# Kernel tuning notes

Hardware: AMD Instinct MI355X
Metric: run time of the kernel (lower is better)

## Reference

```python
import jax, jax.numpy as jnp
import numpy as np

GAMMA = 20.0
GAMMA2 = 10.0
KATZ_FACTOR = 0.999
EPS = 1e-12


def setup_inputs() -> dict:
    key = jax.random.key(0)
    k1, k2 = jax.random.split(key)
    b, n_way, k_shot, q, c, h, w = 32, 5, 5, 75, 640, 5, 5
    support_xf = jax.random.normal(k1, (b, n_way * k_shot, c, h, w), dtype=jnp.float32)
    query_xf = jax.random.normal(k2, (b, q, c, h, w), dtype=jnp.float32)
    return {"support_xf": support_xf, "query_xf": query_xf, "n_way": n_way, "k_shot": k_shot}


def _l2norm(x, axis):
    return x * jax.lax.rsqrt(jnp.sum(x * x, axis=axis, keepdims=True) + EPS)


def reference(support_xf, query_xf, n_way, k_shot):
    b, s, c, h, w = support_xf.shape
    q = query_xf.shape[1]
    hw = h * w
    # prototype support features: mean over shots -> (b, n_way, c, hw)
    sup = support_xf.reshape(b, n_way, k_shot, c, hw).mean(axis=2)
    qry = query_xf.reshape(b, q, c, hw)
    # cosine similarity between every query location and every support location
    sup_n = _l2norm(sup, axis=2)   # (b, n, c, hw)
    qry_n = _l2norm(qry, axis=2)   # (b, q, c, hw)
    # S[b,q,i,n,k]: query pos i vs support (class n, pos k) -> (b*q, M_q, M_s)
    M_q, M_s = hw, n_way * hw
    N = b * q
    S = jnp.einsum('bqci,bnck->bqink', qry_n, sup_n).reshape(N, M_q, M_s)
    # double softmax transition blocks
    T_sq = jax.nn.softmax(GAMMA * S, axis=-1)                    # (N, M_q, M_s)
    T_qs = jax.nn.softmax(GAMMA2 * S.transpose(0, 2, 1), axis=-1)  # (N, M_s, M_q)
    # bipartite block transition matrix T (N, M_s+M_q, M_s+M_q)
    top = jnp.concatenate(
        [jnp.zeros((N, M_s, M_s), S.dtype), T_sq.transpose(0, 2, 1)], axis=-1)
    bot = jnp.concatenate(
        [T_qs.transpose(0, 2, 1), jnp.zeros((N, M_q, M_q), S.dtype)], axis=-1)
    T = jnp.concatenate([top, bot], axis=-2)
    M = M_s + M_q
    eye = jnp.eye(M, dtype=S.dtype)
    ones = jnp.ones((N, M, 1), S.dtype)
    # katz = (inv(I - kT) - I) @ 1 == solve(I - kT, 1) - 1
    katz = (jnp.linalg.solve(eye[None] - KATZ_FACTOR * T, ones) - ones).squeeze(-1)
    kq = katz[:, M_s:]
    ks = katz[:, :M_s]
    katz_query = kq / kq.sum(-1, keepdims=True)
    katz_support = ks / ks.sum(-1, keepdims=True)
    katz_support = katz_support.reshape(b, q, n_way, hw)
    katz_support = katz_support / katz_support.sum(-1, keepdims=True)
    katz_support = katz_support.reshape(b, q, n_way, 1, h, w)
    katz_query = katz_query.reshape(b, q, 1, h, w)
    return (katz_query, katz_support)
```

## Files before the change

kernel.cpp:

```cpp
#include <hip/hip_runtime.h>

namespace {
constexpr int CH = 640, HW = 25, MS = 125;
constexpr int CHW = CH * HW;
constexpr float GAMMA = 20.f, GAMMA2 = 10.f;
constexpr float EPS = 1e-12f;
}

__global__ __launch_bounds__(256)
void prep_sup128_kernel(const float* __restrict__ sup, float* __restrict__ supt) {
  __shared__ __align__(16) float m[CHW];
  __shared__ float inv[HW];
  const int bn = blockIdx.x;
  const int b = bn / 5, n = bn % 5;
  const float* base = sup + ((size_t)b * 25 + n * 5) * CHW;
  for (int idx = threadIdx.x; idx < CHW; idx += 256) {
    float s = 0.f;
    #pragma unroll
    for (int sh = 0; sh < 5; ++sh) s += base[sh * CHW + idx];
    m[idx] = s * 0.2f;
  }
  __syncthreads();
  {
    int i = threadIdx.x >> 3, s8 = threadIdx.x & 7;
    if (i < HW) {
      float p = 0.f;
      for (int c = s8; c < CH; c += 8) { float v = m[c * HW + i]; p += v * v; }
      p += __shfl_xor(p, 1); p += __shfl_xor(p, 2); p += __shfl_xor(p, 4);
      if (s8 == 0) inv[i] = rsqrtf(p + EPS);
    }
  }
  __syncthreads();
  float* ob = supt + (size_t)b * (CH * 128);
  for (int idx = threadIdx.x; idx < CHW; idx += 256) {
    int c = idx / 25, i = idx - c * 25;
    ob[c * 128 + n * 25 + i] = m[idx] * inv[i];
  }
  if (n == 0)
    for (int c = threadIdx.x; c < CH; c += 256) {
      ob[c * 128 + 125] = 0.f; ob[c * 128 + 126] = 0.f; ob[c * 128 + 127] = 0.f;
    }
}

__global__ __launch_bounds__(256)
void prep_sup_kernel(const float* __restrict__ sup, float* __restrict__ sup_t) {
  __shared__ __align__(16) float m[CHW];
  __shared__ float inv[HW];
  const int bn = blockIdx.x;
  const float* base = sup + (size_t)(bn / 5) * (25 * CHW) + (size_t)(bn % 5) * (5 * CHW);
  for (int idx = threadIdx.x; idx < CHW; idx += 256) {
    float s = 0.f;
    #pragma unroll
    for (int sh = 0; sh < 5; ++sh) s += base[sh * CHW + idx];
    m[idx] = s * 0.2f;
  }
  __syncthreads();
  {
    int i = threadIdx.x >> 3, s8 = threadIdx.x & 7;
    if (i < HW) {
      float p = 0.f;
      for (int c = s8; c < CH; c += 8) { float v = m[c * HW + i]; p += v * v; }
      p += __shfl_xor(p, 1); p += __shfl_xor(p, 2); p += __shfl_xor(p, 4);
      if (s8 == 0) inv[i] = rsqrtf(p + EPS);
    }
  }
  __syncthreads();
  float* outp = sup_t + (size_t)bn * CHW;
  for (int idx = threadIdx.x; idx < CHW; idx += 256) {
    int k = idx / CH, c = idx - k * CH;
    outp[idx] = m[c * HW + k] * inv[k];
  }
}

__global__ __launch_bounds__(256)
void gemm_s_kernel(const float* __restrict__ qry, const float* __restrict__ sup128,
                   float* __restrict__ Sout) {
  __shared__ __align__(16) float atile[2][16 * 128];
  __shared__ __align__(16) float btile[2][16 * 128];
  __shared__ float invq_s[128];

  const int tid = threadIdx.x;
  const int wid = tid >> 6, lane = tid & 63;
  const int Bl = (blockIdx.x & 7) * 60 + (blockIdx.x >> 3);
  const int b = Bl / 15, qg = Bl - 15 * b;
  const float* qbase = qry + ((size_t)b * 75 + (size_t)qg * 5) * CHW;
  const float* sb = sup128 + (size_t)b * (CH * 128);
  const int ty = tid >> 4, tx = tid & 15;

  const int row0 = lane;
  const int qq0 = row0 / 25, i0 = row0 - 25 * qq0;
  int row1 = 64 + lane; if (row1 > 124) row1 = 124;
  const int qq1 = row1 / 25, i1 = row1 - 25 * qq1;
  const size_t aoff0 = (size_t)qq0 * CHW + i0;
  const size_t aoff1 = (size_t)qq1 * CHW + i1;

  auto STAGE = [&](int pp, int c0) {
    float* at = atile[pp];
    float* bt = btile[pp];
    #pragma unroll
    for (int rr = 0; rr < 8; ++rr) {
      const int r = 8 * wid + rr;
      const int k = r >> 1;
      const size_t aoff = (r & 1) ? aoff1 : aoff0;
      const float* src = qbase + aoff + (size_t)(c0 + k) * 25;
      __builtin_amdgcn_global_load_lds(
          (const __attribute__((address_space(1))) void*)src,
          (__attribute__((address_space(3))) void*)(at + r * 64), 4, 0, 0);
    }
    #pragma unroll
    for (int jj = 0; jj < 2; ++jj) {
      const int j = 2 * wid + jj;
      const float* src = sb + (size_t)(c0 + 2 * j) * 128 + lane * 4;
      __builtin_amdgcn_global_load_lds(
          (const __attribute__((address_space(1))) void*)src,
          (__attribute__((address_space(3))) void*)(bt + j * 256), 16, 0, 0);
    }
  };

  float acc[2][2][4][4];
  #pragma unroll
  for (int g = 0; g < 2; ++g)
    #pragma unroll
    for (int h = 0; h < 2; ++h)
      #pragma unroll
      for (int u = 0; u < 4; ++u)
        #pragma unroll
        for (int v = 0; v < 4; ++v) acc[g][h][u][v] = 0.f;
  float npart = 0.f;

  STAGE(0, 0);
  asm volatile("s_waitcnt vmcnt(0)" ::: "memory");
  __syncthreads();

  int p = 0;
  for (int t = 0; t < 40; ++t) {
    if (t < 39) STAGE(p ^ 1, 16 * (t + 1));
    const float* at = atile[p];
    const float* bt = btile[p];
    if (tid < MS) {
      #pragma unroll
      for (int k = 0; k < 16; ++k) { float v = at[k * 128 + tid]; npart += v * v; }
    }
    #pragma unroll
    for (int k = 0; k < 16; ++k) {
      const float4 a0 = *(const float4*)&at[k * 128 + 4 * ty];
      const float4 a1 = *(const float4*)&at[k * 128 + 64 + 4 * ty];
      const float4 b0 = *(const float4*)&bt[k * 128 + 4 * tx];
      const float4 b1 = *(const float4*)&bt[k * 128 + 64 + 4 * tx];
      const float ag[2][4] = {{a0.x, a0.y, a0.z, a0.w}, {a1.x, a1.y, a1.z, a1.w}};
      const float bg[2][4] = {{b0.x, b0.y, b0.z, b0.w}, {b1.x, b1.y, b1.z, b1.w}};
      #pragma unroll
      for (int g = 0; g < 2; ++g)
        #pragma unroll
        for (int u = 0; u < 4; ++u)
          #pragma unroll
          for (int h = 0; h < 2; ++h)
            #pragma unroll
            for (int v = 0; v < 4; ++v) acc[g][h][u][v] += ag[g][u] * bg[h][v];
    }
    asm volatile("s_waitcnt vmcnt(0)" ::: "memory");
    __syncthreads();
    p ^= 1;
  }
  if (tid < MS) invq_s[tid] = rsqrtf(npart + EPS);
  __syncthreads();

  float* Sg = Sout + (size_t)(b * 75 + qg * 5) * 3200;
  #pragma unroll
  for (int g = 0; g < 2; ++g)
    #pragma unroll
    for (int u = 0; u < 4; ++u) {
      const int row = g * 64 + 4 * ty + u;
      if (row < MS) {
        const float iv = invq_s[row];
        const int qq = row / 25, r = row - 25 * qq;
        #pragma unroll
        for (int h = 0; h < 2; ++h) {
          float4 val;
          val.x = acc[g][h][u][0] * iv;
          val.y = acc[g][h][u][1] * iv;
          val.z = acc[g][h][u][2] * iv;
          val.w = acc[g][h][u][3] * iv;
          *(float4*)(Sg + (size_t)qq * 3200 + r * 128 + h * 64 + 4 * tx) = val;
        }
      }
    }
}

__global__ __launch_bounds__(256)
void solve_kernel(const float* __restrict__ Sg, float* __restrict__ out) {
  __shared__ float Sld[25 * 131];
  __shared__ float Qm[3125];
  __shared__ double Msol[675];
  __shared__ double xsd[HW];
  __shared__ float kqs[HW];
  __shared__ float ksf[MS];

  const int tid = threadIdx.x;
  const int bq = blockIdx.x;
  const float* src = Sg + (size_t)bq * 3200;
  for (int idx = tid; idx < 3200; idx += 256) {
    const int row = idx >> 7, c = idx & 127;
    Sld[row * 131 + c] = src[idx];
  }
  __syncthreads();

  if (tid < MS) {
    float mx = -1e30f;
    #pragma unroll
    for (int i = 0; i < HW; ++i) mx = fmaxf(mx, Sld[i * 131 + tid]);
    float e[HW]; float sum = 0.f;
    #pragma unroll
    for (int i = 0; i < HW; ++i) { e[i] = __expf(GAMMA2 * (Sld[i * 131 + tid] - mx)); sum += e[i]; }
    float is = 1.f / sum;
    #pragma unroll
    for (int i = 0; i < HW; ++i) Qm[tid * HW + i] = e[i] * is;
  }
  __syncthreads();

  {
    int i = tid >> 3, s8 = tid & 7;
    if (i < HW) {
      float mx = -1e30f;
      for (int j = s8; j < MS; j += 8) mx = fmaxf(mx, Sld[i * 131 + j]);
      mx = fmaxf(mx, __shfl_xor(mx, 1));
      mx = fmaxf(mx, __shfl_xor(mx, 2));
      mx = fmaxf(mx, __shfl_xor(mx, 4));
      float sum = 0.f;
      for (int j = s8; j < MS; j += 8) {
        float e = __expf(GAMMA * (Sld[i * 131 + j] - mx));
        Sld[i * 131 + j] = e; sum += e;
      }
      sum += __shfl_xor(sum, 1); sum += __shfl_xor(sum, 2); sum += __shfl_xor(sum, 4);
      float is = 1.f / sum;
      for (int j = s8; j < MS; j += 8) Sld[i * 131 + j] *= is;
    }
  }
  __syncthreads();

  #pragma unroll
  for (int t = 0; t < 3; ++t) {
    const int pp = tid + 256 * t;
    if (pp < 650) {
      const int i = pp / 26, i2 = pp - 26 * i;
      float s = 0.f;
      if (i2 < 25) {
        for (int j = 0; j < MS; ++j) s += Qm[j * HW + i] * Sld[i2 * 131 + j];
        Msol[i * 27 + i2] = (i == i2 ? 1.0 : 0.0) - 0.998001 * (double)s;
      } else {
        for (int j = 0; j < MS; ++j) s += Qm[j * HW + i];
        Msol[i * 27 + 25] = 1.0 + 0.999 * (double)s;
      }
    }
  }
  __syncthreads();

  for (int k = 0; k < 24; ++k) {
    const double invp = 1.0 / Msol[k * 27 + k];
    const int jj = k + 1 + (tid & 31);
    for (int i = k + 1 + (tid >> 5); i < HW; i += 8) {
      const double f = Msol[i * 27 + k] * invp;
      if (jj <= HW) Msol[i * 27 + jj] -= f * Msol[k * 27 + jj];
    }
    __syncthreads();
  }
  for (int k = 24; k >= 0; --k) {
    const double xk = Msol[k * 27 + 25] / Msol[k * 27 + k];
    if (tid == 0) xsd[k] = xk;
    if (tid < k) Msol[tid * 27 + 25] -= Msol[tid * 27 + k] * xk;
    __syncthreads();
  }

  if (tid < HW) kqs[tid] = (float)(xsd[tid] - 1.0);
  if (tid < MS) {
    float a = 0.f;
    #pragma unroll
    for (int i = 0; i < HW; ++i) a += Sld[i * 131 + tid] * (float)xsd[i];
    ksf[tid] = 0.999f * a;
  }
  __syncthreads();
  if (tid < HW) {
    float s = 0.f;
    #pragma unroll
    for (int i = 0; i < HW; ++i) s += kqs[i];
    out[(size_t)bq * HW + tid] = kqs[tid] / s;
  }
  if (tid < MS) {
    const int n = tid / HW;
    float s = 0.f;
    #pragma unroll
    for (int k2 = 0; k2 < HW; ++k2) s += ksf[n * HW + k2];
    out[60000 + (size_t)bq * MS + tid] = ksf[tid] / s;
  }
}

__global__ __launch_bounds__(256)
void melmask_kernel(const float* __restrict__ qry, const float* __restrict__ sup_t,
                    float* __restrict__ out) {
  __shared__ __align__(16) float pool[4224];
  __shared__ __align__(16) float Sld[3125];
  __shared__ double Msol[675];
  __shared__ double xsd[HW];
  __shared__ float invq_s[128];
  __shared__ float kqs[HW];
  __shared__ float ksf[MS];

  float* atile = pool;
  float* btile = pool + 2112;
  float* Qm    = pool;

  const int tid = threadIdx.x;
  const int Bl = (blockIdx.x & 7) * 60 + (blockIdx.x >> 3);
  const int b = Bl / 15, qg = Bl - 15 * b;
  const float* qbase = qry + ((size_t)b * 75 + (size_t)qg * 5) * CHW;
  const float* sbase = sup_t + (size_t)b * (MS * CH);
  const int ty = tid >> 4, tx = tid & 15;

  float acc[2][2][4][4];
  #pragma unroll
  for (int g = 0; g < 2; ++g)
    #pragma unroll
    for (int h = 0; h < 2; ++h)
      #pragma unroll
      for (int u = 0; u < 4; ++u)
        #pragma unroll
        for (int v = 0; v < 4; ++v) acc[g][h][u][v] = 0.f;
  float npart = 0.f;

  for (int c0 = 0; c0 < CH; c0 += 16) {
    __syncthreads();
    #pragma unroll
    for (int mm = 0; mm < 8; ++mm) {
      int idx = tid + 256 * mm;
      int k = idx >> 7, row = idx & 127;
      float v = 0.f;
      if (row < MS) {
        int qq = row / 25, i = row - 25 * qq;
        v = qbase[(size_t)qq * CHW + (size_t)(c0 + k) * 25 + i];
      }
      atile[k * 132 + row] = v;
    }
    #pragma unroll
    for (int mm = 0; mm < 2; ++mm) {
      int idx = tid + 256 * mm;
      int col = idx >> 2, kq = idx & 3;
      float4 v = make_float4(0.f, 0.f, 0.f, 0.f);
      if (col < MS) v = *(const float4*)(sbase + (size_t)col * CH + c0 + 4 * kq);
      btile[(4 * kq + 0) * 132 + col] = v.x;
      btile[(4 * kq + 1) * 132 + col] = v.y;
      btile[(4 * kq + 2) * 132 + col] = v.z;
      btile[(4 * kq + 3) * 132 + col] = v.w;
    }
    __syncthreads();
    if (tid < MS) {
      #pragma unroll
      for (int k = 0; k < 16; ++k) { float v = atile[k * 132 + tid]; npart += v * v; }
    }
    #pragma unroll
    for (int k = 0; k < 16; ++k) {
      const float4 a0 = *(const float4*)&atile[k * 132 + 4 * ty];
      const float4 a1 = *(const float4*)&atile[k * 132 + 64 + 4 * ty];
      const float4 b0 = *(const float4*)&btile[k * 132 + 4 * tx];
      const float4 b1 = *(const float4*)&btile[k * 132 + 64 + 4 * tx];
      const float ag[2][4] = {{a0.x, a0.y, a0.z, a0.w}, {a1.x, a1.y, a1.z, a1.w}};
      const float bg[2][4] = {{b0.x, b0.y, b0.z, b0.w}, {b1.x, b1.y, b1.z, b1.w}};
      #pragma unroll
      for (int g = 0; g < 2; ++g)
        #pragma unroll
        for (int u = 0; u < 4; ++u)
          #pragma unroll
          for (int h = 0; h < 2; ++h)
            #pragma unroll
            for (int v = 0; v < 4; ++v) acc[g][h][u][v] += ag[g][u] * bg[h][v];
    }
  }
  if (tid < MS) invq_s[tid] = rsqrtf(npart + EPS);
  __syncthreads();

  for (int qq = 0; qq < 5; ++qq) {
    const int bq = b * 75 + qg * 5 + qq;
    const int r0 = qq * 25;
    #pragma unroll
    for (int g = 0; g < 2; ++g)
      #pragma unroll
      for (int u = 0; u < 4; ++u) {
        const int row = g * 64 + 4 * ty + u;
        if (row >= r0 && row < r0 + 25) {
          const int r = row - r0;
          const float iv = invq_s[row];
          #pragma unroll
          for (int h = 0; h < 2; ++h)
            #pragma unroll
            for (int v = 0; v < 4; ++v) {
              const int col = h * 64 + 4 * tx + v;
              if (col < MS) Sld[r * MS + col] = acc[g][h][u][v] * iv;
            }
        }
      }
    __syncthreads();
    if (tid < MS) {
      float mx = -1e30f;
      #pragma unroll
      for (int i = 0; i < HW; ++i) mx = fmaxf(mx, Sld[i * MS + tid]);
      float e[HW]; float sum = 0.f;
      #pragma unroll
      for (int i = 0; i < HW; ++i) { e[i] = __expf(GAMMA2 * (Sld[i * MS + tid] - mx)); sum += e[i]; }
      float is = 1.f / sum;
      #pragma unroll
      for (int i = 0; i < HW; ++i) Qm[tid * HW + i] = e[i] * is;
    }
    __syncthreads();
    {
      int i = tid >> 3, s8 = tid & 7;
      if (i < HW) {
        float mx = -1e30f;
        for (int j = s8; j < MS; j += 8) mx = fmaxf(mx, Sld[i * MS + j]);
        mx = fmaxf(mx, __shfl_xor(mx, 1));
        mx = fmaxf(mx, __shfl_xor(mx, 2));
        mx = fmaxf(mx, __shfl_xor(mx, 4));
        float sum = 0.f;
        for (int j = s8; j < MS; j += 8) {
          float e = __expf(GAMMA * (Sld[i * MS + j] - mx));
          Sld[i * MS + j] = e; sum += e;
        }
        sum += __shfl_xor(sum, 1); sum += __shfl_xor(sum, 2); sum += __shfl_xor(sum, 4);
        float is = 1.f / sum;
        for (int j = s8; j < MS; j += 8) Sld[i * MS + j] *= is;
      }
    }
    __syncthreads();
    float* P = Sld;
    #pragma unroll
    for (int t = 0; t < 3; ++t) {
      const int pp = tid + 256 * t;
      if (pp < 650) {
        const int i = pp / 26, i2 = pp - 26 * i;
        float s = 0.f;
        if (i2 < 25) {
          for (int j = 0; j < MS; ++j) s += Qm[j * HW + i] * P[i2 * MS + j];
          Msol[i * 27 + i2] = (i == i2 ? 1.0 : 0.0) - 0.998001 * (double)s;
        } else {
          for (int j = 0; j < MS; ++j) s += Qm[j * HW + i];
          Msol[i * 27 + 25] = 1.0 + 0.999 * (double)s;
        }
      }
    }
    __syncthreads();
    for (int k = 0; k < 24; ++k) {
      const double invp = 1.0 / Msol[k * 27 + k];
      const int jj = k + 1 + (tid & 31);
      for (int i = k + 1 + (tid >> 5); i < HW; i += 8) {
        const double f = Msol[i * 27 + k] * invp;
        if (jj <= HW) Msol[i * 27 + jj] -= f * Msol[k * 27 + jj];
      }
      __syncthreads();
    }
    for (int k = 24; k >= 0; --k) {
      const double xk = Msol[k * 27 + 25] / Msol[k * 27 + k];
      if (tid == 0) xsd[k] = xk;
      if (tid < k) Msol[tid * 27 + 25] -= Msol[tid * 27 + k] * xk;
      __syncthreads();
    }
    if (tid < HW) kqs[tid] = (float)(xsd[tid] - 1.0);
    if (tid < MS) {
      float a = 0.f;
      #pragma unroll
      for (int i = 0; i < HW; ++i) a += P[i * MS + tid] * (float)xsd[i];
      ksf[tid] = 0.999f * a;
    }
    __syncthreads();
    if (tid < HW) {
      float s = 0.f;
      #pragma unroll
      for (int i = 0; i < HW; ++i) s += kqs[i];
      out[(size_t)bq * HW + tid] = kqs[tid] / s;
    }
    if (tid < MS) {
      const int n = tid / HW;
      float s = 0.f;
      #pragma unroll
      for (int k2 = 0; k2 < HW; ++k2) s += ksf[n * HW + k2];
      out[60000 + (size_t)bq * MS + tid] = ksf[tid] / s;
    }
    __syncthreads();
  }
}

extern "C" void kernel_launch(void* const* d_in, const int* in_sizes, int n_in,
                              void* d_out, int out_size, void* d_ws, size_t ws_size,
                              hipStream_t stream) {
  const float* sup = (const float*)d_in[0];
  const float* qry = (const float*)d_in[1];
  float* outp = (float*)d_out;
  const size_t sup128_bytes = (size_t)32 * CH * 128 * 4;
  const size_t sg_bytes = (size_t)2400 * 3200 * 4;
  if (ws_size >= sup128_bytes + sg_bytes) {
    float* sup128 = (float*)d_ws;
    float* Sg = (float*)((char*)d_ws + sup128_bytes);
    prep_sup128_kernel<<<160, 256, 0, stream>>>(sup, sup128);
    gemm_s_kernel<<<480, 256, 0, stream>>>(qry, sup128, Sg);
    solve_kernel<<<2400, 256, 0, stream>>>(Sg, outp);
  } else {
    float* sup_t = (float*)d_ws;
    prep_sup_kernel<<<160, 256, 0, stream>>>(sup, sup_t);
    melmask_kernel<<<480, 256, 0, stream>>>(qry, sup_t, outp);
  }
}
```

Baseline: 243.1 us.

## Split GEMM reduction over channels into two halves to double block count

The similarity GEMM is split along the 640-channel reduction into two halves, so 960 blocks run instead of 480. Each half writes its partial S and partial query-norm sums to separate workspace buffers. The solve kernel then adds the two partials and applies the inverse norm before the existing softmax and solve steps. This is meant to raise occupancy on a GPU with many CUs, at the cost of extra workspace traffic and a larger workspace requirement. The old fused melmask fallback is removed and the non-split gemm path becomes the fallback.

```diff
diff --git a/kernel.cpp b/kernel.cpp
--- a/kernel.cpp
+++ b/kernel.cpp
@@ -43,33 +43,118 @@
 }
 
 __global__ __launch_bounds__(256)
-void prep_sup_kernel(const float* __restrict__ sup, float* __restrict__ sup_t) {
-  __shared__ __align__(16) float m[CHW];
-  __shared__ float inv[HW];
-  const int bn = blockIdx.x;
-  const float* base = sup + (size_t)(bn / 5) * (25 * CHW) + (size_t)(bn % 5) * (5 * CHW);
-  for (int idx = threadIdx.x; idx < CHW; idx += 256) {
-    float s = 0.f;
-    #pragma unroll
-    for (int sh = 0; sh < 5; ++sh) s += base[sh * CHW + idx];
-    m[idx] = s * 0.2f;
-  }
-  __syncthreads();
-  {
-    int i = threadIdx.x >> 3, s8 = threadIdx.x & 7;
-    if (i < HW) {
-      float p = 0.f;
-      for (int c = s8; c < CH; c += 8) { float v = m[c * HW + i]; p += v * v; }
-      p += __shfl_xor(p, 1); p += __shfl_xor(p, 2); p += __shfl_xor(p, 4);
-      if (s8 == 0) inv[i] = rsqrtf(p + EPS);
-    }
-  }
-  __syncthreads();
-  float* outp = sup_t + (size_t)bn * CHW;
-  for (int idx = threadIdx.x; idx < CHW; idx += 256) {
-    int k = idx / CH, c = idx - k * CH;
-    outp[idx] = m[c * HW + k] * inv[k];
-  }
+void gemm_ks_kernel(const float* __restrict__ qry, const float* __restrict__ sup128,
+                    float* __restrict__ Sg1, float* __restrict__ Sg2,
+                    float* __restrict__ npws) {
+  __shared__ __align__(16) float atile[2][16 * 128];
+  __shared__ __align__(16) float btile[2][16 * 128];
+
+  const int tid = threadIdx.x;
+  const int wid = tid >> 6, lane = tid & 63;
+  const int x = blockIdx.x & 7, rr0 = blockIdx.x >> 3;
+  const int Bl = x * 120 + rr0;
+  const int group = Bl >> 1, half = Bl & 1;
+  const int b = group / 15, qg = group - 15 * b;
+  const float* qbase = qry + ((size_t)b * 75 + (size_t)qg * 5) * CHW;
+  const float* sb = sup128 + (size_t)b * (CH * 128);
+  const int ty = tid >> 4, tx = tid & 15;
+  const int kbase = half * 320;
+
+  const int row0 = lane;
+  const int qq0 = row0 / 25, i0 = row0 - 25 * qq0;
+  int row1 = 64 + lane; if (row1 > 124) row1 = 124;
+  const int qq1 = row1 / 25, i1 = row1 - 25 * qq1;
+  const size_t aoff0 = (size_t)qq0 * CHW + i0;
+  const size_t aoff1 = (size_t)qq1 * CHW + i1;
+
+  auto STAGE = [&](int pp, int c0) {
+    float* at = atile[pp];
+    float* bt = btile[pp];
+    #pragma unroll
+    for (int rr = 0; rr < 8; ++rr) {
+      const int r = 8 * wid + rr;
+      const int k = r >> 1;
+      const size_t aoff = (r & 1) ? aoff1 : aoff0;
+      const float* src = qbase + aoff + (size_t)(c0 + k) * 25;
+      __builtin_amdgcn_global_load_lds(
+          (const __attribute__((address_space(1))) void*)src,
+          (__attribute__((address_space(3))) void*)(at + r * 64), 4, 0, 0);
+    }
+    #pragma unroll
+    for (int jj = 0; jj < 2; ++jj) {
+      const int j = 2 * wid + jj;
+      const float* src = sb + (size_t)(c0 + 2 * j) * 128 + lane * 4;
+      __builtin_amdgcn_global_load_lds(
+          (const __attribute__((address_space(1))) void*)src,
+          (__attribute__((address_space(3))) void*)(bt + j * 256), 16, 0, 0);
+    }
+  };
+
+  float acc[2][2][4][4];
+  #pragma unroll
+  for (int g = 0; g < 2; ++g)
+    #pragma unroll
+    for (int h = 0; h < 2; ++h)
+      #pragma unroll
+      for (int u = 0; u < 4; ++u)
+        #pragma unroll
+        for (int v = 0; v < 4; ++v) acc[g][h][u][v] = 0.f;
+  float npart = 0.f;
+
+  STAGE(0, kbase);
+  asm volatile("s_waitcnt vmcnt(0)" ::: "memory");
+  __syncthreads();
+
+  int p = 0;
+  for (int t = 0; t < 20; ++t) {
+    if (t < 19) STAGE(p ^ 1, kbase + 16 * (t + 1));
+    const float* at = atile[p];
+    const float* bt = btile[p];
+    if (tid < MS) {
+      #pragma unroll
+      for (int k = 0; k < 16; ++k) { float v = at[k * 128 + tid]; npart += v * v; }
+    }
+    #pragma unroll
+    for (int k = 0; k < 16; ++k) {
+      const float4 a0 = *(const float4*)&at[k * 128 + 4 * ty];
+      const float4 a1 = *(const float4*)&at[k * 128 + 64 + 4 * ty];
+      const float4 b0 = *(const float4*)&bt[k * 128 + 4 * tx];
+      const float4 b1 = *(const float4*)&bt[k * 128 + 64 + 4 * tx];
+      const float ag[2][4] = {{a0.x, a0.y, a0.z, a0.w}, {a1.x, a1.y, a1.z, a1.w}};
+      const float bg[2][4] = {{b0.x, b0.y, b0.z, b0.w}, {b1.x, b1.y, b1.z, b1.w}};
+      #pragma unroll
+      for (int g = 0; g < 2; ++g)
+        #pragma unroll
+        for (int u = 0; u < 4; ++u)
+          #pragma unroll
+          for (int h = 0; h < 2; ++h)
+            #pragma unroll
+            for (int v = 0; v < 4; ++v) acc[g][h][u][v] += ag[g][u] * bg[h][v];
+    }
+    asm volatile("s_waitcnt vmcnt(0)" ::: "memory");
+    __syncthreads();
+    p ^= 1;
+  }
+
+  if (tid < MS) npws[(size_t)(group * 2 + half) * 128 + tid] = npart;
+
+  float* Sg = (half ? Sg2 : Sg1) + (size_t)(group * 5) * 3200;
+  #pragma unroll
+  for (int g = 0; g < 2; ++g)
+    #pragma unroll
+    for (int u = 0; u < 4; ++u) {
+      const int row = g * 64 + 4 * ty + u;
+      if (row < MS) {
+        const int qq = row / 25, r = row - 25 * qq;
+        #pragma unroll
+        for (int h = 0; h < 2; ++h) {
+          float4 val;
+          val.x = acc[g][h][u][0]; val.y = acc[g][h][u][1];
+          val.z = acc[g][h][u][2]; val.w = acc[g][h][u][3];
+          *(float4*)(Sg + (size_t)qq * 3200 + r * 128 + h * 64 + 4 * tx) = val;
+        }
+      }
+    }
 }
 
 __global__ __launch_bounds__(256)
@@ -187,24 +272,9 @@
     }
 }
 
-__global__ __launch_bounds__(256)
-void solve_kernel(const float* __restrict__ Sg, float* __restrict__ out) {
-  __shared__ float Sld[25 * 131];
-  __shared__ float Qm[3125];
-  __shared__ double Msol[675];
-  __shared__ double xsd[HW];
-  __shared__ float kqs[HW];
-  __shared__ float ksf[MS];
-
-  const int tid = threadIdx.x;
-  const int bq = blockIdx.x;
-  const float* src = Sg + (size_t)bq * 3200;
-  for (int idx = tid; idx < 3200; idx += 256) {
-    const int row = idx >> 7, c = idx & 127;
-    Sld[row * 131 + c] = src[idx];
-  }
-  __syncthreads();
-
+__device__ __forceinline__
+void solve_body(float* Sld, float* Qm, double* Msol, double* xsd,
+                float* kqs, float* ksf, int tid, int bq, float* out) {
   if (tid < MS) {
     float mx = -1e30f;
     #pragma unroll
@@ -295,195 +365,53 @@
 }
 
 __global__ __launch_bounds__(256)
-void melmask_kernel(const float* __restrict__ qry, const float* __restrict__ sup_t,
-                    float* __restrict__ out) {
-  __shared__ __align__(16) float pool[4224];
-  __shared__ __align__(16) float Sld[3125];
+void solve_ks_kernel(const float* __restrict__ Sg1, const float* __restrict__ Sg2,
+                     const float* __restrict__ npws, float* __restrict__ out) {
+  __shared__ float Sld[25 * 131];
+  __shared__ float Qm[3125];
   __shared__ double Msol[675];
   __shared__ double xsd[HW];
-  __shared__ float invq_s[128];
   __shared__ float kqs[HW];
   __shared__ float ksf[MS];
-
-  float* atile = pool;
-  float* btile = pool + 2112;
-  float* Qm    = pool;
+  __shared__ float ivrow[32];
 
   const int tid = threadIdx.x;
-  const int Bl = (blockIdx.x & 7) * 60 + (blockIdx.x >> 3);
-  const int b = Bl / 15, qg = Bl - 15 * b;
-  const float* qbase = qry + ((size_t)b * 75 + (size_t)qg * 5) * CHW;
-  const float* sbase = sup_t + (size_t)b * (MS * CH);
-  const int ty = tid >> 4, tx = tid & 15;
-
-  float acc[2][2][4][4];
-  #pragma unroll
-  for (int g = 0; g < 2; ++g)
-    #pragma unroll
-    for (int h = 0; h < 2; ++h)
-      #pragma unroll
-      for (int u = 0; u < 4; ++u)
-        #pragma unroll
-        for (int v = 0; v < 4; ++v) acc[g][h][u][v] = 0.f;
-  float npart = 0.f;
-
-  for (int c0 = 0; c0 < CH; c0 += 16) {
-    __syncthreads();
-    #pragma unroll
-    for (int mm = 0; mm < 8; ++mm) {
-      int idx = tid + 256 * mm;
-      int k = idx >> 7, row = idx & 127;
-      float v = 0.f;
-      if (row < MS) {
-        int qq = row / 25, i = row - 25 * qq;
-        v = qbase[(size_t)qq * CHW + (size_t)(c0 + k) * 25 + i];
-      }
-      atile[k * 132 + row] = v;
-    }
-    #pragma unroll
-    for (int mm = 0; mm < 2; ++mm) {
-      int idx = tid + 256 * mm;
-      int col = idx >> 2, kq = idx & 3;
-      float4 v = make_float4(0.f, 0.f, 0.f, 0.f);
-      if (col < MS) v = *(const float4*)(sbase + (size_t)col * CH + c0 + 4 * kq);
-      btile[(4 * kq + 0) * 132 + col] = v.x;
-      btile[(4 * kq + 1) * 132 + col] = v.y;
-      btile[(4 * kq + 2) * 132 + col] = v.z;
-      btile[(4 * kq + 3) * 132 + col] = v.w;
-    }
-    __syncthreads();
-    if (tid < MS) {
-      #pragma unroll
-      for (int k = 0; k < 16; ++k) { float v = atile[k * 132 + tid]; npart += v * v; }
-    }
-    #pragma unroll
-    for (int k = 0; k < 16; ++k) {
-      const float4 a0 = *(const float4*)&atile[k * 132 + 4 * ty];
-      const float4 a1 = *(const float4*)&atile[k * 132 + 64 + 4 * ty];
-      const float4 b0 = *(const float4*)&btile[k * 132 + 4 * tx];
-      const float4 b1 = *(const float4*)&btile[k * 132 + 64 + 4 * tx];
-      const float ag[2][4] = {{a0.x, a0.y, a0.z, a0.w}, {a1.x, a1.y, a1.z, a1.w}};
-      const float bg[2][4] = {{b0.x, b0.y, b0.z, b0.w}, {b1.x, b1.y, b1.z, b1.w}};
-      #pragma unroll
-      for (int g = 0; g < 2; ++g)
-        #pragma unroll
-        for (int u = 0; u < 4; ++u)
-          #pragma unroll
-          for (int h = 0; h < 2; ++h)
-            #pragma unroll
-            for (int v = 0; v < 4; ++v) acc[g][h][u][v] += ag[g][u] * bg[h][v];
-    }
-  }
-  if (tid < MS) invq_s[tid] = rsqrtf(npart + EPS);
-  __syncthreads();
-
-  for (int qq = 0; qq < 5; ++qq) {
-    const int bq = b * 75 + qg * 5 + qq;
-    const int r0 = qq * 25;
-    #pragma unroll
-    for (int g = 0; g < 2; ++g)
-      #pragma unroll
-      for (int u = 0; u < 4; ++u) {
-        const int row = g * 64 + 4 * ty + u;
-        if (row >= r0 && row < r0 + 25) {
-          const int r = row - r0;
-          const float iv = invq_s[row];
-          #pragma unroll
-          for (int h = 0; h < 2; ++h)
-            #pragma unroll
-            for (int v = 0; v < 4; ++v) {
-              const int col = h * 64 + 4 * tx + v;
-              if (col < MS) Sld[r * MS + col] = acc[g][h][u][v] * iv;
-            }
-        }
-      }
-    __syncthreads();
-    if (tid < MS) {
-      float mx = -1e30f;
-      #pragma unroll
-      for (int i = 0; i < HW; ++i) mx = fmaxf(mx, Sld[i * MS + tid]);
-      float e[HW]; float sum = 0.f;
-      #pragma unroll
-      for (int i = 0; i < HW; ++i) { e[i] = __expf(GAMMA2 * (Sld[i * MS + tid] - mx)); sum += e[i]; }
-      float is = 1.f / sum;
-      #pragma unroll
-      for (int i = 0; i < HW; ++i) Qm[tid * HW + i] = e[i] * is;
-    }
-    __syncthreads();
-    {
-      int i = tid >> 3, s8 = tid & 7;
-      if (i < HW) {
-        float mx = -1e30f;
-        for (int j = s8; j < MS; j += 8) mx = fmaxf(mx, Sld[i * MS + j]);
-        mx = fmaxf(mx, __shfl_xor(mx, 1));
-        mx = fmaxf(mx, __shfl_xor(mx, 2));
-        mx = fmaxf(mx, __shfl_xor(mx, 4));
-        float sum = 0.f;
-        for (int j = s8; j < MS; j += 8) {
-          float e = __expf(GAMMA * (Sld[i * MS + j] - mx));
-          Sld[i * MS + j] = e; sum += e;
-        }
-        sum += __shfl_xor(sum, 1); sum += __shfl_xor(sum, 2); sum += __shfl_xor(sum, 4);
-        float is = 1.f / sum;
-        for (int j = s8; j < MS; j += 8) Sld[i * MS + j] *= is;
-      }
-    }
-    __syncthreads();
-    float* P = Sld;
-    #pragma unroll
-    for (int t = 0; t < 3; ++t) {
-      const int pp = tid + 256 * t;
-      if (pp < 650) {
-        const int i = pp / 26, i2 = pp - 26 * i;
-        float s = 0.f;
-        if (i2 < 25) {
-          for (int j = 0; j < MS; ++j) s += Qm[j * HW + i] * P[i2 * MS + j];
-          Msol[i * 27 + i2] = (i == i2 ? 1.0 : 0.0) - 0.998001 * (double)s;
-        } else {
-          for (int j = 0; j < MS; ++j) s += Qm[j * HW + i];
-          Msol[i * 27 + 25] = 1.0 + 0.999 * (double)s;
-        }
-      }
-    }
-    __syncthreads();
-    for (int k = 0; k < 24; ++k) {
-      const double invp = 1.0 / Msol[k * 27 + k];
-      const int jj = k + 1 + (tid & 31);
-      for (int i = k + 1 + (tid >> 5); i < HW; i += 8) {
-        const double f = Msol[i * 27 + k] * invp;
-        if (jj <= HW) Msol[i * 27 + jj] -= f * Msol[k * 27 + jj];
-      }
-      __syncthreads();
-    }
-    for (int k = 24; k >= 0; --k) {
-      const double xk = Msol[k * 27 + 25] / Msol[k * 27 + k];
-      if (tid == 0) xsd[k] = xk;
-      if (tid < k) Msol[tid * 27 + 25] -= Msol[tid * 27 + k] * xk;
-      __syncthreads();
-    }
-    if (tid < HW) kqs[tid] = (float)(xsd[tid] - 1.0);
-    if (tid < MS) {
-      float a = 0.f;
-      #pragma unroll
-      for (int i = 0; i < HW; ++i) a += P[i * MS + tid] * (float)xsd[i];
-      ksf[tid] = 0.999f * a;
-    }
-    __syncthreads();
-    if (tid < HW) {
-      float s = 0.f;
-      #pragma unroll
-      for (int i = 0; i < HW; ++i) s += kqs[i];
-      out[(size_t)bq * HW + tid] = kqs[tid] / s;
-    }
-    if (tid < MS) {
-      const int n = tid / HW;
-      float s = 0.f;
-      #pragma unroll
-      for (int k2 = 0; k2 < HW; ++k2) s += ksf[n * HW + k2];
-      out[60000 + (size_t)bq * MS + tid] = ksf[tid] / s;
-    }
-    __syncthreads();
-  }
+  const int bq = blockIdx.x;
+  const int g5 = bq / 5, qq = bq - 5 * g5;
+  if (tid < HW) {
+    const float n1 = npws[(size_t)(g5 * 2 + 0) * 128 + qq * 25 + tid];
+    const float n2 = npws[(size_t)(g5 * 2 + 1) * 128 + qq * 25 + tid];
+    ivrow[tid] = rsqrtf(n1 + n2 + EPS);
+  }
+  __syncthreads();
+  const float* s1 = Sg1 + (size_t)bq * 3200;
+  const float* s2 = Sg2 + (size_t)bq * 3200;
+  for (int idx = tid; idx < 3200; idx += 256) {
+    const int row = idx >> 7, c = idx & 127;
+    Sld[row * 131 + c] = (s1[idx] + s2[idx]) * ivrow[row];
+  }
+  __syncthreads();
+  solve_body(Sld, Qm, Msol, xsd, kqs, ksf, tid, bq, out);
+}
+
+__global__ __launch_bounds__(256)
+void solve_kernel(const float* __restrict__ Sg, float* __restrict__ out) {
+  __shared__ float Sld[25 * 131];
+  __shared__ float Qm[3125];
+  __shared__ double Msol[675];
+  __shared__ double xsd[HW];
+  __shared__ float kqs[HW];
+  __shared__ float ksf[MS];
+
+  const int tid = threadIdx.x;
+  const int bq = blockIdx.x;
+  const float* src = Sg + (size_t)bq * 3200;
+  for (int idx = tid; idx < 3200; idx += 256) {
+    const int row = idx >> 7, c = idx & 127;
+    Sld[row * 131 + c] = src[idx];
+  }
+  __syncthreads();
+  solve_body(Sld, Qm, Msol, xsd, kqs, ksf, tid, bq, out);
 }
 
 extern "C" void kernel_launch(void* const* d_in, const int* in_sizes, int n_in,
@@ -494,15 +422,18 @@
   float* outp = (float*)d_out;
   const size_t sup128_bytes = (size_t)32 * CH * 128 * 4;
   const size_t sg_bytes = (size_t)2400 * 3200 * 4;
-  if (ws_size >= sup128_bytes + sg_bytes) {
-    float* sup128 = (float*)d_ws;
+  const size_t np_bytes = (size_t)480 * 2 * 128 * 4;
+  float* sup128 = (float*)d_ws;
+  prep_sup128_kernel<<<160, 256, 0, stream>>>(sup, sup128);
+  if (ws_size >= sup128_bytes + 2 * sg_bytes + np_bytes) {
+    float* Sg1 = (float*)((char*)d_ws + sup128_bytes);
+    float* Sg2 = (float*)((char*)d_ws + sup128_bytes + sg_bytes);
+    float* npws = (float*)((char*)d_ws + sup128_bytes + 2 * sg_bytes);
+    gemm_ks_kernel<<<960, 256, 0, stream>>>(qry, sup128, Sg1, Sg2, npws);
+    solve_ks_kernel<<<2400, 256, 0, stream>>>(Sg1, Sg2, npws, outp);
+  } else {
     float* Sg = (float*)((char*)d_ws + sup128_bytes);
-    prep_sup128_kernel<<<160, 256, 0, stream>>>(sup, sup128);
     gemm_s_kernel<<<480, 256, 0, stream>>>(qry, sup128, Sg);
     solve_kernel<<<2400, 256, 0, stream>>>(Sg, outp);
-  } else {
-    float* sup_t = (float*)d_ws;
-    prep_sup_kernel<<<160, 256, 0, stream>>>(sup, sup_t);
-    melmask_kernel<<<480, 256, 0, stream>>>(qry, sup_t, outp);
-  }
-}
+  }
+}
```

Result: slower. 306.4 us (+26.0%).
